# Kernel optimization log

Measured on AMD Instinct MI355X. Metric: run time of the kernel, lower is better.

Reference implementation:

```python
import jax, jax.numpy as jnp
import numpy as np

EMB = 1024
HEADS = 8
SEQ = 4096
LN_EPS = 1e-5


def _layernorm(x, g, b):
    mu = jnp.mean(x, axis=-1, keepdims=True)
    var = jnp.mean(jnp.square(x - mu), axis=-1, keepdims=True)
    return (x - mu) * jax.lax.rsqrt(var + LN_EPS) * g + b


def setup_inputs() -> dict:
    key = jax.random.key(0)
    ks = jax.random.split(key, 12)
    s = 1.0 / np.sqrt(EMB)
    sz = 1.0 / np.sqrt(EMB * HEADS)
    return {
        "history": jax.random.normal(ks[0], (SEQ, EMB), jnp.float32),
        "embdding": jax.random.normal(ks[1], (SEQ, EMB), jnp.float32),
        # per-head Linear weights, torch layout [out, in], stacked over heads
        "Wq_w": jax.random.uniform(ks[2], (HEADS, EMB, EMB), jnp.float32, -s, s),
        "Wq_b": jax.random.uniform(ks[3], (HEADS, EMB), jnp.float32, -s, s),
        "Wk_w": jax.random.uniform(ks[4], (HEADS, EMB, EMB), jnp.float32, -s, s),
        "Wk_b": jax.random.uniform(ks[5], (HEADS, EMB), jnp.float32, -s, s),
        "Wv_w": jax.random.uniform(ks[6], (HEADS, EMB, EMB), jnp.float32, -s, s),
        "Wv_b": jax.random.uniform(ks[7], (HEADS, EMB), jnp.float32, -s, s),
        "Wz_w": jax.random.uniform(ks[8], (EMB, EMB * HEADS), jnp.float32, -sz, sz),
        "Wz_b": jax.random.uniform(ks[9], (EMB,), jnp.float32, -sz, sz),
        "ln1_g": jnp.ones((EMB,), jnp.float32),
        "ln1_b": jnp.zeros((EMB,), jnp.float32),
        "Wf_w": jax.random.uniform(ks[10], (EMB, EMB), jnp.float32, -s, s),
        "Wf_b": jax.random.uniform(ks[11], (EMB,), jnp.float32, -s, s),
        "ln2_g": jnp.ones((EMB,), jnp.float32),
        "ln2_b": jnp.zeros((EMB,), jnp.float32),
    }


def reference(history, embdding, Wq_w, Wq_b, Wk_w, Wk_b, Wv_w, Wv_b,
              Wz_w, Wz_b, ln1_g, ln1_b, Wf_w, Wf_b, ln2_g, ln2_b):
    S, E = embdding.shape
    H = Wq_w.shape[0]
    # per-head linears (torch: y = x @ W.T + b), batched over heads
    Q = jnp.einsum('se,hfe->hsf', embdding, Wq_w) + Wq_b[:, None, :]  # [H,S,E]
    K = jnp.einsum('se,hfe->hsf', embdding, Wk_w) + Wk_b[:, None, :]
    V = jnp.einsum('se,hfe->hsf', history, Wv_w) + Wv_b[:, None, :]
    # K^T @ Q -> [H, E, E], softmax over dim=1 of the 2D matrix == last axis here
    scores = jnp.einsum('hse,hsf->hef', K, Q) / jnp.sqrt(jnp.asarray(E, Q.dtype))
    A = jax.nn.softmax(scores, axis=-1)  # [H,E,E]
    Zh = jnp.einsum('hse,hef->hsf', V, A)  # [H,S,E]
    Z = jnp.transpose(Zh, (1, 0, 2)).reshape(S, H * E)  # cat(dim=1) in head order
    O = Z @ Wz_w.T + Wz_b  # [S,E]
    LN1 = _layernorm(O, ln1_g, ln1_b) + embdding
    FN = LN1 @ Wf_w.T + Wf_b
    LN2 = _layernorm(FN, ln2_g, ln2_b) + LN1
    return LN2
```

## Files before the change

### kernel.cpp

```cpp
#include <hip/hip_runtime.h>


constexpr int EMB = 1024;
constexpr int SEQ = 4096;
constexpr int NH  = 8;

using f32x4  = __attribute__((ext_vector_type(4))) float;
using bf16x8 = __attribute__((ext_vector_type(8))) __bf16;
using us8    = __attribute__((ext_vector_type(8))) unsigned short;

#define GLOAD_LDS16(g, l) __builtin_amdgcn_global_load_lds(                 \
    (const __attribute__((address_space(1))) void*)(g),                     \
    (__attribute__((address_space(3))) void*)(l), 16, 0, 0)

__device__ inline unsigned short f2bf(float x) {
  unsigned int u = __float_as_uint(x);
  u += 0x7FFFu + ((u >> 16) & 1u);
  return (unsigned short)(u >> 16);
}
__device__ inline float bf2f(unsigned short h) {
  return __uint_as_float(((unsigned int)h) << 16);
}

__global__ __launch_bounds__(256) void mega_cvt_k(
    const float* __restrict__ Wk, const float* __restrict__ Wq,
    const float* __restrict__ hist, const float* __restrict__ Wz,
    const float* __restrict__ Wf, const float* __restrict__ emb,
    const float* __restrict__ Wv, const float* __restrict__ xbar,
    unsigned short* __restrict__ Wkb, unsigned short* __restrict__ Wqb,
    unsigned short* __restrict__ Yb, unsigned short* __restrict__ Wzb,
    unsigned short* __restrict__ Wfb, unsigned short* __restrict__ XT,
    unsigned short* __restrict__ WvT,
    float* __restrict__ u, float* __restrict__ v) {
  __shared__ float red[4];
  __shared__ float tile[32][33];
  const int b = blockIdx.x, tid = threadIdx.x;

  if (b < 16384) {
    const float* src = (b < 8192) ? Wk : Wq;
    unsigned short* dst = (b < 8192) ? Wkb : Wqb;
    float* dot = (b < 8192) ? u : v;
    int row = b & 8191;
    float4 x  = ((const float4*)(src + (size_t)row * EMB))[tid];
    float4 xb = ((const float4*)xbar)[tid];
    ushort4 o; o.x = f2bf(x.x); o.y = f2bf(x.y); o.z = f2bf(x.z); o.w = f2bf(x.w);
    ((ushort4*)(dst + (size_t)row * EMB))[tid] = o;
    float s = x.x * xb.x + x.y * xb.y + x.z * xb.z + x.w * xb.w;
    int lane = tid & 63, w = tid >> 6;
#pragma unroll
    for (int off = 32; off; off >>= 1) s += __shfl_down(s, off);
    if (lane == 0) red[w] = s;
    __syncthreads();
    if (tid == 0) dot[row] = red[0] + red[1] + red[2] + red[3];
  } else if (b < 29696) {
    const float* src; unsigned short* dst; int row;
    if (b < 20480)      { src = hist; dst = Yb;  row = b - 16384; }
    else if (b < 28672) { src = Wz;   dst = Wzb; row = b - 20480; }
    else                { src = Wf;   dst = Wfb; row = b - 28672; }
    float4 x = ((const float4*)(src + (size_t)row * EMB))[tid];
    ushort4 o; o.x = f2bf(x.x); o.y = f2bf(x.y); o.z = f2bf(x.z); o.w = f2bf(x.w);
    ((ushort4*)(dst + (size_t)row * EMB))[tid] = o;
  } else {
    const float* src; unsigned short* dst; int rows, c0, r0;
    if (b < 33792) {
      int tt = b - 29696;
      src = emb; dst = XT; rows = SEQ;
      c0 = (tt & 31) * 32; r0 = (tt >> 5) * 32;
    } else {
      int t2 = b - 33792;
      int z = t2 >> 10, tt = t2 & 1023;
      src = Wv + (size_t)z * EMB * EMB; dst = WvT + (size_t)z * EMB * EMB;
      rows = EMB;
      c0 = (tt & 31) * 32; r0 = (tt >> 5) * 32;
    }
    int tx = tid & 31, ty = tid >> 5;
#pragma unroll
    for (int k = 0; k < 4; ++k) {
      int r = ty + k * 8;
      tile[r][tx] = src[(size_t)(r0 + r) * EMB + c0 + tx];
    }
    __syncthreads();
#pragma unroll
    for (int k = 0; k < 4; ++k) {
      int r = ty + k * 8;
      dst[(size_t)(c0 + r) * rows + r0 + tx] = f2bf(tile[tx][r]);
    }
  }
}

__global__ __launch_bounds__(256) void colsum_part_k(const float* __restrict__ X,
                                                     float* __restrict__ part) {
  int e = blockIdx.x * 256 + threadIdx.x;
  int y = blockIdx.y;
  float s = 0.f;
  for (int r = y * 128; r < y * 128 + 128; ++r) s += X[(size_t)r * EMB + e];
  part[y * EMB + e] = s;
}
__global__ __launch_bounds__(256) void colsum_red_k(const float* __restrict__ part,
                                                    float* __restrict__ xbar) {
  int e = blockIdx.x * 256 + threadIdx.x;
  float s = 0.f;
  for (int y = 0; y < 32; ++y) s += part[y * EMB + e];
  xbar[e] = s;
}

__global__ __launch_bounds__(256) void dvec_k(const unsigned short* __restrict__ Wzb,
                                              const float* __restrict__ bz,
                                              const float* __restrict__ c,
                                              float* __restrict__ d) {
  __shared__ float sb[4];
  int g = blockIdx.x, tid = threadIdx.x;
  const unsigned short* row = Wzb + (size_t)g * (NH * EMB);
  float s = 0.f;
#pragma unroll
  for (int p = 0; p < 4; ++p) {
    int i = p * 256 + tid;
    us8 w = ((const us8*)row)[i];
    float4 c0 = ((const float4*)c)[i * 2];
    float4 c1 = ((const float4*)c)[i * 2 + 1];
    s += bf2f(w[0]) * c0.x + bf2f(w[1]) * c0.y + bf2f(w[2]) * c0.z + bf2f(w[3]) * c0.w;
    s += bf2f(w[4]) * c1.x + bf2f(w[5]) * c1.y + bf2f(w[6]) * c1.z + bf2f(w[7]) * c1.w;
  }
  int lane = tid & 63, w = tid >> 6;
#pragma unroll
  for (int off = 32; off; off >>= 1) s += __shfl_down(s, off);
  if (lane == 0) sb[w] = s;
  __syncthreads();
  if (tid == 0) d[g] = bz[g] + sb[0] + sb[1] + sb[2] + sb[3];
}

__global__ __launch_bounds__(256) void mred_tr_k(const unsigned short* __restrict__ Mp,
                                                 unsigned short* __restrict__ MT) {
  __shared__ float t[32][33];
  int g0 = blockIdx.x * 32, e0 = blockIdx.y * 32;
  int tx = threadIdx.x & 31, ty = threadIdx.x >> 5;
#pragma unroll
  for (int k = 0; k < 4; ++k) {
    int e = e0 + ty + k * 8;
    float s = 0.f;
#pragma unroll
    for (int h = 0; h < NH; ++h)
      s += bf2f(Mp[((size_t)h << 20) + (size_t)e * EMB + g0 + tx]);
    t[ty + k * 8][tx] = s;
  }
  __syncthreads();
#pragma unroll
  for (int k = 0; k < 4; ++k) {
    int r = ty + k * 8;
    MT[(size_t)(g0 + r) * EMB + e0 + tx] = f2bf(t[tx][r]);
  }
}

__global__ __launch_bounds__(256) void gram_red_k(const unsigned short* __restrict__ Gp,
                                                  unsigned short* __restrict__ Gbf) {
  int i = blockIdx.x * 256 + threadIdx.x;
  float4 s = {0.f, 0.f, 0.f, 0.f};
#pragma unroll
  for (int z = 0; z < 8; ++z) {
    ushort4 v = ((const ushort4*)(Gp + (size_t)z * EMB * EMB))[i];
    s.x += bf2f(v.x); s.y += bf2f(v.y); s.z += bf2f(v.z); s.w += bf2f(v.w);
  }
  ushort4 o; o.x = f2bf(s.x); o.y = f2bf(s.y); o.z = f2bf(s.z); o.w = f2bf(s.w);
  ((ushort4*)Gbf)[i] = o;
}

__global__ __launch_bounds__(256) void colstat1_k(const float* __restrict__ ScT,
                                                  float* __restrict__ m_part,
                                                  float* __restrict__ s_part) {
  int col = blockIdx.x * 256 + threadIdx.x;
  int rc = blockIdx.y, h = blockIdx.z;
  const float* base = ScT + ((size_t)h * EMB + rc * 64) * EMB + col;
  float m = -1e30f, s = 0.f;
#pragma unroll 4
  for (int r = 0; r < 64; ++r) {
    float x = base[(size_t)r * EMB];
    float nm = fmaxf(m, x);
    s = s * __expf(m - nm) + __expf(x - nm);
    m = nm;
  }
  m_part[((size_t)h * 16 + rc) * EMB + col] = m;
  s_part[((size_t)h * 16 + rc) * EMB + col] = s;
}

__global__ __launch_bounds__(256) void colstat2_k(const float* __restrict__ m_part,
                                                  const float* __restrict__ s_part,
                                                  float* __restrict__ mfin,
                                                  float* __restrict__ isfin) {
  int i = blockIdx.x * 256 + threadIdx.x;
  int h = i >> 10, col = i & 1023;
  float M = -1e30f, S = 0.f;
#pragma unroll
  for (int c = 0; c < 16; ++c) {
    float m = m_part[((size_t)h * 16 + c) * EMB + col];
    float s = s_part[((size_t)h * 16 + c) * EMB + col];
    float nm = fmaxf(M, m);
    S = S * __expf(M - nm) + s * __expf(m - nm);
    M = nm;
  }
  mfin[i] = M;
  isfin[i] = 1.0f / S;
}

__global__ __launch_bounds__(256) void at_cvec_k(const float* __restrict__ ScT,
                                                 const float* __restrict__ mfin,
                                                 const float* __restrict__ isfin,
                                                 const float* __restrict__ bv,
                                                 unsigned short* __restrict__ AT,
                                                 float* __restrict__ cbuf) {
  __shared__ float sb[4];
  int f = blockIdx.x, h = blockIdx.y, tid = threadIdx.x;
  size_t rowoff = ((size_t)h * EMB + f) * EMB;
  float4 x  = ((const float4*)(ScT + rowoff))[tid];
  float4 m  = ((const float4*)(mfin + (size_t)h * EMB))[tid];
  float4 is = ((const float4*)(isfin + (size_t)h * EMB))[tid];
  float4 b  = ((const float4*)(bv + (size_t)h * EMB))[tid];
  float a0 = __expf(x.x - m.x) * is.x;
  float a1 = __expf(x.y - m.y) * is.y;
  float a2 = __expf(x.z - m.z) * is.z;
  float a3 = __expf(x.w - m.w) * is.w;
  ushort4 o; o.x = f2bf(a0); o.y = f2bf(a1); o.z = f2bf(a2); o.w = f2bf(a3);
  ((ushort4*)(AT + rowoff))[tid] = o;
  float s = a0 * b.x + a1 * b.y + a2 * b.z + a3 * b.w;
  int lane = tid & 63, w = tid >> 6;
#pragma unroll
  for (int off = 32; off; off >>= 1) s += __shfl_down(s, off);
  if (lane == 0) sb[w] = s;
  __syncthreads();
  if (tid == 0) cbuf[h * EMB + f] = sb[0] + sb[1] + sb[2] + sb[3];
}

__global__ __launch_bounds__(256) void layernorm_k(const float* __restrict__ Xin,
                                                   const float* __restrict__ resid,
                                                   const float* __restrict__ gw,
                                                   const float* __restrict__ bw,
                                                   float* __restrict__ outf,
                                                   unsigned short* __restrict__ outb) {
  __shared__ float sb[16];
  int row = blockIdx.x, tid = threadIdx.x;
  float4 v = ((const float4*)(Xin + (size_t)row * EMB))[tid];
  float s = v.x + v.y + v.z + v.w;
  float q = v.x * v.x + v.y * v.y + v.z * v.z + v.w * v.w;
  int lane = tid & 63, w = tid >> 6;
#pragma unroll
  for (int off = 32; off; off >>= 1) { s += __shfl_down(s, off); q += __shfl_down(q, off); }
  if (lane == 0) { sb[w] = s; sb[8 + w] = q; }
  __syncthreads();
  float mu  = (sb[0] + sb[1] + sb[2] + sb[3]) * (1.0f / EMB);
  float var = (sb[8] + sb[9] + sb[10] + sb[11]) * (1.0f / EMB) - mu * mu;
  float rs = rsqrtf(var + 1e-5f);
  float4 rv = ((const float4*)(resid + (size_t)row * EMB))[tid];
  float4 gv = ((const float4*)gw)[tid];
  float4 bv = ((const float4*)bw)[tid];
  float o0 = (v.x - mu) * rs * gv.x + bv.x + rv.x;
  float o1 = (v.y - mu) * rs * gv.y + bv.y + rv.y;
  float o2 = (v.z - mu) * rs * gv.z + bv.z + rv.z;
  float o3 = (v.w - mu) * rs * gv.w + bv.w + rv.w;
  float4 ov; ov.x = o0; ov.y = o1; ov.z = o2; ov.w = o3;
  ((float4*)(outf + (size_t)row * EMB))[tid] = ov;
  if (outb) {
    ushort4 ob; ob.x = f2bf(o0); ob.y = f2bf(o1); ob.z = f2bf(o2); ob.w = f2bf(o3);
    ((ushort4*)(outb + (size_t)row * EMB))[tid] = ob;
  }
}

template <int MODE>
__global__ __launch_bounds__(256) void gemm_nt(const unsigned short* __restrict__ A,
                                               const unsigned short* __restrict__ B,
                                               void* __restrict__ Cout,
                                               int K, int lda, int ldb, int ldc,
                                               long long aZ, long long bZ, long long cZ,
                                               const float* __restrict__ e0,
                                               const float* __restrict__ e1,
                                               const float* __restrict__ e2,
                                               const float* __restrict__ e3) {
  const int z = blockIdx.z;
  A += (size_t)z * aZ;
  B += (size_t)z * bZ;
  const int tid = threadIdx.x;
  const int lane = tid & 63, wid = tid >> 6;
  const int wm = wid >> 1, wn = wid & 1;
  const int row0 = blockIdx.x * 128, col0 = blockIdx.y * 128;

  __shared__ __align__(16) unsigned short As[2][128 * 64];
  __shared__ __align__(16) unsigned short Bs[2][128 * 64];

  f32x4 acc[4][4] = {};
  const int lrow = lane & 15, kg = lane >> 4;
  const int lr = lane >> 3;
  const int lc = (lane & 7) * 8;

  auto stage = [&](int buf, int k0) {
#pragma unroll
    for (int c = 0; c < 4; ++c) {
      int chunk = wid * 4 + c;
      int r = chunk * 8 + lr;
      GLOAD_LDS16(A + (size_t)(row0 + r) * lda + k0 + lc, &As[buf][chunk * 512]);
      GLOAD_LDS16(B + (size_t)(col0 + r) * ldb + k0 + lc, &Bs[buf][chunk * 512]);
    }
  };

  stage(0, 0);
  __syncthreads();

  const int nt = K >> 6;
  for (int t = 0; t < nt; ++t) {
    const int cur = t & 1;
    if (t + 1 < nt) stage(cur ^ 1, (t + 1) << 6);
#pragma unroll
    for (int ks = 0; ks < 2; ++ks) {
      bf16x8 a[4], b[4];
      int koff = ks * 32 + kg * 8;
#pragma unroll
      for (int i = 0; i < 4; ++i)
        a[i] = *(const bf16x8*)&As[cur][(wm * 64 + i * 16 + lrow) * 64 + koff];
#pragma unroll
      for (int j = 0; j < 4; ++j)
        b[j] = *(const bf16x8*)&Bs[cur][(wn * 64 + j * 16 + lrow) * 64 + koff];
#pragma unroll
      for (int i = 0; i < 4; ++i)
#pragma unroll
        for (int j = 0; j < 4; ++j)
          acc[i][j] = __builtin_amdgcn_mfma_f32_16x16x32_bf16(a[i], b[j], acc[i][j], 0, 0, 0);
    }
    __syncthreads();
  }

  const int rb = (lane >> 4) * 4, cc = lane & 15;
#pragma unroll
  for (int i = 0; i < 4; ++i) {
#pragma unroll
    for (int j = 0; j < 4; ++j) {
#pragma unroll
      for (int r = 0; r < 4; ++r) {
        int m = row0 + wm * 64 + i * 16 + rb + r;
        int n = col0 + wn * 64 + j * 16 + cc;
        float val = acc[i][j][r];
        size_t off = (size_t)z * cZ + (size_t)m * ldc + n;
        if (MODE == 0) {
          ((float*)Cout)[off] = val;
        } else if (MODE == 1) {
          ((unsigned short*)Cout)[off] = f2bf(val);
        } else if (MODE == 3) {
          ((float*)Cout)[off] = val + e0[n];
        } else if (MODE == 4) {
          float bq = e0[z * EMB + m], uu = e1[z * EMB + n];
          float bk = e2[z * EMB + n], vv = e3[z * EMB + m];
          ((float*)Cout)[off] = (val + bq * (uu + (float)SEQ * bk) + vv * bk) * (1.0f / 32.0f);
        }
      }
    }
  }
}

extern "C" void kernel_launch(void* const* d_in, const int* in_sizes, int n_in,
                              void* d_out, int out_size, void* d_ws, size_t ws_size,
                              hipStream_t stream) {
  const float* history = (const float*)d_in[0];
  const float* emb     = (const float*)d_in[1];
  const float* Wq_w = (const float*)d_in[2];
  const float* Wq_b = (const float*)d_in[3];
  const float* Wk_w = (const float*)d_in[4];
  const float* Wk_b = (const float*)d_in[5];
  const float* Wv_w = (const float*)d_in[6];
  const float* Wv_b = (const float*)d_in[7];
  const float* Wz_w = (const float*)d_in[8];
  const float* Wz_b = (const float*)d_in[9];
  const float* ln1_g = (const float*)d_in[10];
  const float* ln1_b = (const float*)d_in[11];
  const float* Wf_w = (const float*)d_in[12];
  const float* Wf_b = (const float*)d_in[13];
  const float* ln2_g = (const float*)d_in[14];
  const float* ln2_b = (const float*)d_in[15];

  char* ws = (char*)d_ws;
  const size_t MB = 1024ull * 1024ull;
  unsigned short* XT  = (unsigned short*)(ws + 0);
  unsigned short* Ybf = (unsigned short*)(ws + 8 * MB);
  unsigned short* Wkb = (unsigned short*)(ws + 16 * MB);
  unsigned short* Wqb = (unsigned short*)(ws + 32 * MB);
  unsigned short* WvT = (unsigned short*)(ws + 48 * MB);
  unsigned short* Wzb = (unsigned short*)(ws + 64 * MB);
  unsigned short* Wfb = (unsigned short*)(ws + 80 * MB);
  unsigned short* Gbf = (unsigned short*)(ws + 82 * MB);
  float* xpart = (float*)(ws + 84 * MB);
  float* xbar  = (float*)(ws + 84 * MB + 160 * 1024);
  float* ubuf  = (float*)(ws + 84 * MB + 192 * 1024);
  float* vbuf  = (float*)(ws + 84 * MB + 256 * 1024);
  float* cbuf  = (float*)(ws + 84 * MB + 320 * 1024);
  float* dbuf  = (float*)(ws + 84 * MB + 384 * 1024);
  unsigned short* Tbf = (unsigned short*)(ws + 85 * MB);
  float* Sc  = (float*)(ws + 101 * MB);
  char*  St  = ws + 133 * MB;
  unsigned short* ATb = (unsigned short*)(ws + 149 * MB);
  unsigned short* MTb = (unsigned short*)(ws + 165 * MB);
  float* m_part = (float*)(St);
  float* s_part = (float*)(St + 512 * 1024);
  float* mfin   = (float*)(St + 1024 * 1024);
  float* isfin  = (float*)(St + 1056 * 1024);
  unsigned short* Gp = (unsigned short*)Sc;
  unsigned short* Cbf  = Tbf;
  unsigned short* Mp = (unsigned short*)Sc;
  float* Obuf = (float*)St;
  float* LN1  = (float*)ATb;
  unsigned short* LN1b = XT;
  float* FN   = (float*)Tbf;

  colsum_part_k<<<dim3(4, 32), 256, 0, stream>>>(emb, xpart);
  colsum_red_k<<<dim3(4), 256, 0, stream>>>(xpart, xbar);

  mega_cvt_k<<<dim3(41984), 256, 0, stream>>>(Wk_w, Wq_w, history, Wz_w, Wf_w,
                                              emb, Wv_w, xbar,
                                              Wkb, Wqb, Ybf, Wzb, Wfb, XT, WvT,
                                              ubuf, vbuf);

  gemm_nt<1><<<dim3(8, 8, 8), 256, 0, stream>>>(XT, XT, Gp, 512, SEQ, SEQ, EMB,
                                                512, 512, (long long)EMB * EMB,
                                                nullptr, nullptr, nullptr, nullptr);
  gram_red_k<<<dim3(EMB * EMB / 4 / 256), 256, 0, stream>>>(Gp, Gbf);
  gemm_nt<1><<<dim3(8, 8, NH), 256, 0, stream>>>(Wqb, Gbf, Tbf, EMB, EMB, EMB, EMB,
                                                 (long long)EMB * EMB, 0, (long long)EMB * EMB,
                                                 nullptr, nullptr, nullptr, nullptr);
  gemm_nt<4><<<dim3(8, 8, NH), 256, 0, stream>>>(Tbf, Wkb, Sc, EMB, EMB, EMB, EMB,
                                                 (long long)EMB * EMB, (long long)EMB * EMB,
                                                 (long long)EMB * EMB, Wq_b, ubuf, Wk_b, vbuf);
  colstat1_k<<<dim3(4, 16, NH), 256, 0, stream>>>(Sc, m_part, s_part);
  colstat2_k<<<dim3(32), 256, 0, stream>>>(m_part, s_part, mfin, isfin);
  at_cvec_k<<<dim3(EMB, NH), 256, 0, stream>>>(Sc, mfin, isfin, Wv_b, ATb, cbuf);
  gemm_nt<1><<<dim3(8, 8, NH), 256, 0, stream>>>(WvT, ATb, Cbf, EMB, EMB, EMB, EMB,
                                                 (long long)EMB * EMB, (long long)EMB * EMB,
                                                 (long long)EMB * EMB,
                                                 nullptr, nullptr, nullptr, nullptr);
  gemm_nt<1><<<dim3(8, 8, NH), 256, 0, stream>>>(Cbf, Wzb, Mp, EMB, EMB, NH * EMB, EMB,
                                                 (long long)EMB * EMB, (long long)EMB,
                                                 (long long)EMB * EMB,
                                                 nullptr, nullptr, nullptr, nullptr);
  mred_tr_k<<<dim3(EMB / 32, EMB / 32), 256, 0, stream>>>(Mp, MTb);
  dvec_k<<<dim3(EMB), 256, 0, stream>>>(Wzb, Wz_b, cbuf, dbuf);
  gemm_nt<3><<<dim3(SEQ / 128, 8, 1), 256, 0, stream>>>(Ybf, MTb, Obuf, EMB, EMB, EMB, EMB,
                                                        0, 0, 0, dbuf, nullptr, nullptr, nullptr);
  layernorm_k<<<dim3(SEQ), 256, 0, stream>>>(Obuf, emb, ln1_g, ln1_b, LN1, LN1b);
  gemm_nt<3><<<dim3(SEQ / 128, 8, 1), 256, 0, stream>>>(LN1b, Wfb, FN, EMB, EMB, EMB, EMB,
                                                        0, 0, 0, Wf_b, nullptr, nullptr, nullptr);
  layernorm_k<<<dim3(SEQ), 256, 0, stream>>>(FN, LN1, ln2_g, ln2_b, (float*)d_out, nullptr);
}
```

Before: 301.8 us.

## Remap GEMM blocks across XCDs, stage bf16 epilogue in LDS, widen convert tiles

GEMM launches now use a flat 1D grid, with the block index remapped so that consecutive tiles land on the same XCD (an 8-way round-robin swizzle). This is meant to improve L2 reuse of the shared A/B panels. The bf16-output GEMM epilogue now writes through LDS so global stores are 16-byte vectors instead of scattered 2-byte stores. The conversion kernel handles 4096 elements per block for the row copies and uses 64x64 transposes with float4 loads and ushort4 stores, which cuts the block count and makes memory access wider. The costs are extra LDS traffic and a barrier in the epilogue, plus integer index arithmetic.

```diff
diff --git a/kernel.cpp b/kernel.cpp
--- a/kernel.cpp
+++ b/kernel.cpp
@@ -21,6 +21,10 @@
 __device__ inline float bf2f(unsigned short h) {
   return __uint_as_float(((unsigned int)h) << 16);
 }
+
+constexpr int NB_DOT = 16384;
+constexpr int NB_ROW = 3328;
+constexpr int NB_XT  = 1024;
 
 __global__ __launch_bounds__(256) void mega_cvt_k(
     const float* __restrict__ Wk, const float* __restrict__ Wq,
@@ -33,10 +37,10 @@
     unsigned short* __restrict__ WvT,
     float* __restrict__ u, float* __restrict__ v) {
   __shared__ float red[4];
-  __shared__ float tile[32][33];
+  __shared__ float tileT[64][65];
   const int b = blockIdx.x, tid = threadIdx.x;
 
-  if (b < 16384) {
+  if (b < NB_DOT) {
     const float* src = (b < 8192) ? Wk : Wq;
     unsigned short* dst = (b < 8192) ? Wkb : Wqb;
     float* dot = (b < 8192) ? u : v;
@@ -52,38 +56,49 @@
     if (lane == 0) red[w] = s;
     __syncthreads();
     if (tid == 0) dot[row] = red[0] + red[1] + red[2] + red[3];
-  } else if (b < 29696) {
-    const float* src; unsigned short* dst; int row;
-    if (b < 20480)      { src = hist; dst = Yb;  row = b - 16384; }
-    else if (b < 28672) { src = Wz;   dst = Wzb; row = b - 20480; }
-    else                { src = Wf;   dst = Wfb; row = b - 28672; }
-    float4 x = ((const float4*)(src + (size_t)row * EMB))[tid];
-    ushort4 o; o.x = f2bf(x.x); o.y = f2bf(x.y); o.z = f2bf(x.z); o.w = f2bf(x.w);
-    ((ushort4*)(dst + (size_t)row * EMB))[tid] = o;
+  } else if (b < NB_DOT + NB_ROW) {
+    size_t f0 = (size_t)(b - NB_DOT) * 4096;
+    const float* src; unsigned short* dst; size_t loc;
+    if (f0 < 4096ull * 1024) { src = hist; dst = Yb;  loc = f0; }
+    else if (f0 < 12288ull * 1024) { src = Wz; dst = Wzb; loc = f0 - 4096ull * 1024; }
+    else { src = Wf; dst = Wfb; loc = f0 - 12288ull * 1024; }
+#pragma unroll
+    for (int p = 0; p < 4; ++p) {
+      int i = p * 256 + tid;
+      float4 x = ((const float4*)(src + loc))[i];
+      ushort4 o; o.x = f2bf(x.x); o.y = f2bf(x.y); o.z = f2bf(x.z); o.w = f2bf(x.w);
+      ((ushort4*)(dst + loc))[i] = o;
+    }
   } else {
-    const float* src; unsigned short* dst; int rows, c0, r0;
-    if (b < 33792) {
-      int tt = b - 29696;
-      src = emb; dst = XT; rows = SEQ;
-      c0 = (tt & 31) * 32; r0 = (tt >> 5) * 32;
+    int tb = b - (NB_DOT + NB_ROW);
+    const float* src; unsigned short* dst; int R, r0, c0;
+    if (tb < NB_XT) {
+      src = emb; dst = XT; R = SEQ;
+      r0 = (tb >> 4) * 64; c0 = (tb & 15) * 64;
     } else {
-      int t2 = b - 33792;
-      int z = t2 >> 10, tt = t2 & 1023;
+      int t2 = tb - NB_XT, z = t2 >> 8, tt = t2 & 255;
       src = Wv + (size_t)z * EMB * EMB; dst = WvT + (size_t)z * EMB * EMB;
-      rows = EMB;
-      c0 = (tt & 31) * 32; r0 = (tt >> 5) * 32;
-    }
-    int tx = tid & 31, ty = tid >> 5;
-#pragma unroll
-    for (int k = 0; k < 4; ++k) {
-      int r = ty + k * 8;
-      tile[r][tx] = src[(size_t)(r0 + r) * EMB + c0 + tx];
+      R = EMB;
+      r0 = (tt >> 4) * 64; c0 = (tt & 15) * 64;
+    }
+    int tx = tid & 15, ty = tid >> 4;
+#pragma unroll
+    for (int p = 0; p < 4; ++p) {
+      int ir = p * 16 + ty;
+      float4 x = *(const float4*)(src + (size_t)(r0 + ir) * EMB + c0 + tx * 4);
+      tileT[tx * 4 + 0][ir] = x.x; tileT[tx * 4 + 1][ir] = x.y;
+      tileT[tx * 4 + 2][ir] = x.z; tileT[tx * 4 + 3][ir] = x.w;
     }
     __syncthreads();
 #pragma unroll
-    for (int k = 0; k < 4; ++k) {
-      int r = ty + k * 8;
-      dst[(size_t)(c0 + r) * rows + r0 + tx] = f2bf(tile[tx][r]);
+    for (int p = 0; p < 4; ++p) {
+      int orow = p * 16 + ty;
+      ushort4 o;
+      o.x = f2bf(tileT[orow][tx * 4 + 0]);
+      o.y = f2bf(tileT[orow][tx * 4 + 1]);
+      o.z = f2bf(tileT[orow][tx * 4 + 2]);
+      o.w = f2bf(tileT[orow][tx * 4 + 3]);
+      *(ushort4*)(dst + (size_t)(c0 + orow) * R + r0 + tx * 4) = o;
     }
   }
 }
@@ -269,17 +284,22 @@
                                                void* __restrict__ Cout,
                                                int K, int lda, int ldb, int ldc,
                                                long long aZ, long long bZ, long long cZ,
+                                               int nx, int ny,
                                                const float* __restrict__ e0,
                                                const float* __restrict__ e1,
                                                const float* __restrict__ e2,
                                                const float* __restrict__ e3) {
-  const int z = blockIdx.z;
+  const int q = gridDim.x >> 3;
+  const int wg = (blockIdx.x & 7) * q + (blockIdx.x >> 3);
+  const int bx = wg % nx;
+  const int by = (wg / nx) % ny;
+  const int z  = wg / (nx * ny);
   A += (size_t)z * aZ;
   B += (size_t)z * bZ;
   const int tid = threadIdx.x;
   const int lane = tid & 63, wid = tid >> 6;
   const int wm = wid >> 1, wn = wid & 1;
-  const int row0 = blockIdx.x * 128, col0 = blockIdx.y * 128;
+  const int row0 = bx * 128, col0 = by * 128;
 
   __shared__ __align__(16) unsigned short As[2][128 * 64];
   __shared__ __align__(16) unsigned short Bs[2][128 * 64];
@@ -326,26 +346,43 @@
   }
 
   const int rb = (lane >> 4) * 4, cc = lane & 15;
-#pragma unroll
-  for (int i = 0; i < 4; ++i) {
-#pragma unroll
-    for (int j = 0; j < 4; ++j) {
-#pragma unroll
-      for (int r = 0; r < 4; ++r) {
-        int m = row0 + wm * 64 + i * 16 + rb + r;
-        int n = col0 + wn * 64 + j * 16 + cc;
-        float val = acc[i][j][r];
-        size_t off = (size_t)z * cZ + (size_t)m * ldc + n;
-        if (MODE == 0) {
-          ((float*)Cout)[off] = val;
-        } else if (MODE == 1) {
-          ((unsigned short*)Cout)[off] = f2bf(val);
-        } else if (MODE == 3) {
-          ((float*)Cout)[off] = val + e0[n];
-        } else if (MODE == 4) {
-          float bq = e0[z * EMB + m], uu = e1[z * EMB + n];
-          float bk = e2[z * EMB + n], vv = e3[z * EMB + m];
-          ((float*)Cout)[off] = (val + bq * (uu + (float)SEQ * bk) + vv * bk) * (1.0f / 32.0f);
+  if (MODE == 1) {
+    unsigned short* Cs = &As[0][0];
+#pragma unroll
+    for (int i = 0; i < 4; ++i)
+#pragma unroll
+      for (int j = 0; j < 4; ++j)
+#pragma unroll
+        for (int r = 0; r < 4; ++r)
+          Cs[(wm * 64 + i * 16 + rb + r) * 128 + wn * 64 + j * 16 + cc] =
+              f2bf(acc[i][j][r]);
+    __syncthreads();
+    unsigned short* Cg = (unsigned short*)Cout + (size_t)z * cZ;
+#pragma unroll
+    for (int p = 0; p < 8; ++p) {
+      int idx = p * 256 + tid;
+      int row = idx >> 4, col = (idx & 15) * 8;
+      *(us8*)(Cg + (size_t)(row0 + row) * ldc + col0 + col) =
+          *(const us8*)&Cs[row * 128 + col];
+    }
+  } else {
+#pragma unroll
+    for (int i = 0; i < 4; ++i) {
+#pragma unroll
+      for (int j = 0; j < 4; ++j) {
+#pragma unroll
+        for (int r = 0; r < 4; ++r) {
+          int m = row0 + wm * 64 + i * 16 + rb + r;
+          int n = col0 + wn * 64 + j * 16 + cc;
+          float val = acc[i][j][r];
+          size_t off = (size_t)z * cZ + (size_t)m * ldc + n;
+          if (MODE == 3) {
+            ((float*)Cout)[off] = val + e0[n];
+          } else {
+            float bq = e0[z * EMB + m], uu = e1[z * EMB + n];
+            float bk = e2[z * EMB + n], vv = e3[z * EMB + m];
+            ((float*)Cout)[off] = (val + bq * (uu + (float)SEQ * bk) + vv * bk) * (1.0f / 32.0f);
+          }
         }
       }
     }
@@ -408,38 +445,41 @@
   colsum_part_k<<<dim3(4, 32), 256, 0, stream>>>(emb, xpart);
   colsum_red_k<<<dim3(4), 256, 0, stream>>>(xpart, xbar);
 
-  mega_cvt_k<<<dim3(41984), 256, 0, stream>>>(Wk_w, Wq_w, history, Wz_w, Wf_w,
+  mega_cvt_k<<<dim3(22784), 256, 0, stream>>>(Wk_w, Wq_w, history, Wz_w, Wf_w,
                                               emb, Wv_w, xbar,
                                               Wkb, Wqb, Ybf, Wzb, Wfb, XT, WvT,
                                               ubuf, vbuf);
 
-  gemm_nt<1><<<dim3(8, 8, 8), 256, 0, stream>>>(XT, XT, Gp, 512, SEQ, SEQ, EMB,
-                                                512, 512, (long long)EMB * EMB,
-                                                nullptr, nullptr, nullptr, nullptr);
+  gemm_nt<1><<<dim3(512), 256, 0, stream>>>(XT, XT, Gp, 512, SEQ, SEQ, EMB,
+                                            512, 512, (long long)EMB * EMB, 8, 8,
+                                            nullptr, nullptr, nullptr, nullptr);
   gram_red_k<<<dim3(EMB * EMB / 4 / 256), 256, 0, stream>>>(Gp, Gbf);
-  gemm_nt<1><<<dim3(8, 8, NH), 256, 0, stream>>>(Wqb, Gbf, Tbf, EMB, EMB, EMB, EMB,
-                                                 (long long)EMB * EMB, 0, (long long)EMB * EMB,
-                                                 nullptr, nullptr, nullptr, nullptr);
-  gemm_nt<4><<<dim3(8, 8, NH), 256, 0, stream>>>(Tbf, Wkb, Sc, EMB, EMB, EMB, EMB,
-                                                 (long long)EMB * EMB, (long long)EMB * EMB,
-                                                 (long long)EMB * EMB, Wq_b, ubuf, Wk_b, vbuf);
+  gemm_nt<1><<<dim3(512), 256, 0, stream>>>(Wqb, Gbf, Tbf, EMB, EMB, EMB, EMB,
+                                            (long long)EMB * EMB, 0, (long long)EMB * EMB, 8, 8,
+                                            nullptr, nullptr, nullptr, nullptr);
+  gemm_nt<4><<<dim3(512), 256, 0, stream>>>(Tbf, Wkb, Sc, EMB, EMB, EMB, EMB,
+                                            (long long)EMB * EMB, (long long)EMB * EMB,
+                                            (long long)EMB * EMB, 8, 8,
+                                            Wq_b, ubuf, Wk_b, vbuf);
   colstat1_k<<<dim3(4, 16, NH), 256, 0, stream>>>(Sc, m_part, s_part);
   colstat2_k<<<dim3(32), 256, 0, stream>>>(m_part, s_part, mfin, isfin);
   at_cvec_k<<<dim3(EMB, NH), 256, 0, stream>>>(Sc, mfin, isfin, Wv_b, ATb, cbuf);
-  gemm_nt<1><<<dim3(8, 8, NH), 256, 0, stream>>>(WvT, ATb, Cbf, EMB, EMB, EMB, EMB,
-                                                 (long long)EMB * EMB, (long long)EMB * EMB,
-                                                 (long long)EMB * EMB,
-                                                 nullptr, nullptr, nullptr, nullptr);
-  gemm_nt<1><<<dim3(8, 8, NH), 256, 0, stream>>>(Cbf, Wzb, Mp, EMB, EMB, NH * EMB, EMB,
-                                                 (long long)EMB * EMB, (long long)EMB,
-                                                 (long long)EMB * EMB,
-                                                 nullptr, nullptr, nullptr, nullptr);
+  gemm_nt<1><<<dim3(512), 256, 0, stream>>>(WvT, ATb, Cbf, EMB, EMB, EMB, EMB,
+                                            (long long)EMB * EMB, (long long)EMB * EMB,
+                                            (long long)EMB * EMB, 8, 8,
+                                            nullptr, nullptr, nullptr, nullptr);
+  gemm_nt<1><<<dim3(512), 256, 0, stream>>>(Cbf, Wzb, Mp, EMB, EMB, NH * EMB, EMB,
+                                            (long long)EMB * EMB, (long long)EMB,
+                                            (long long)EMB * EMB, 8, 8,
+                                            nullptr, nullptr, nullptr, nullptr);
   mred_tr_k<<<dim3(EMB / 32, EMB / 32), 256, 0, stream>>>(Mp, MTb);
   dvec_k<<<dim3(EMB), 256, 0, stream>>>(Wzb, Wz_b, cbuf, dbuf);
-  gemm_nt<3><<<dim3(SEQ / 128, 8, 1), 256, 0, stream>>>(Ybf, MTb, Obuf, EMB, EMB, EMB, EMB,
-                                                        0, 0, 0, dbuf, nullptr, nullptr, nullptr);
+  gemm_nt<3><<<dim3(256), 256, 0, stream>>>(Ybf, MTb, Obuf, EMB, EMB, EMB, EMB,
+                                            0, 0, 0, 32, 8,
+                                            dbuf, nullptr, nullptr, nullptr);
   layernorm_k<<<dim3(SEQ), 256, 0, stream>>>(Obuf, emb, ln1_g, ln1_b, LN1, LN1b);
-  gemm_nt<3><<<dim3(SEQ / 128, 8, 1), 256, 0, stream>>>(LN1b, Wfb, FN, EMB, EMB, EMB, EMB,
-                                                        0, 0, 0, Wf_b, nullptr, nullptr, nullptr);
+  gemm_nt<3><<<dim3(256), 256, 0, stream>>>(LN1b, Wfb, FN, EMB, EMB, EMB, EMB,
+                                            0, 0, 0, 32, 8,
+                                            Wf_b, nullptr, nullptr, nullptr);
   layernorm_k<<<dim3(SEQ), 256, 0, stream>>>(FN, LN1, ln2_g, ln2_b, (float*)d_out, nullptr);
 }
```

Result: no change. 303.2 us (+0.5%).
